# Kernel tuning notes

Measured on AMD Instinct MI355X. Metric: run time of the kernel, lower is better.

Reference implementation:

```python
import jax, jax.numpy as jnp
import numpy as np

C = 512
H_HEADS = 8
CTX_D = 768
GEO_D = 512
FFN_D = 4 * C
EPS = 1e-5


def _layernorm(x, g, b):
    mu = jnp.mean(x, axis=-1, keepdims=True)
    var = jnp.mean((x - mu) ** 2, axis=-1, keepdims=True)
    return (x - mu) * jax.lax.rsqrt(var + EPS) * g + b


def _cross_attn(x, ctx, Wq, Wk, Wv, Wo, bo, h):
    # x: (B, N, C), ctx: (B, S, Dctx)
    b, n, _ = x.shape
    s = ctx.shape[1]
    inner = Wq.shape[1]
    d = inner // h
    q = (x @ Wq).reshape(b, n, h, d)
    k = (ctx @ Wk).reshape(b, s, h, d)
    v = (ctx @ Wv).reshape(b, s, h, d)
    sim = jnp.einsum('bihd,bjhd->bhij', q, k) * (d ** -0.5)
    attn = jax.nn.softmax(sim, axis=-1)
    out = jnp.einsum('bhij,bjhd->bihd', attn, v).reshape(b, n, inner)
    return out @ Wo + bo


def setup_inputs() -> dict:
    key = jax.random.key(0)
    ks = jax.random.split(key, 24)
    std = lambda fan_in: 1.0 / np.sqrt(fan_in)
    inp = {
        'x': jax.random.normal(ks[0], (4, C, 64, 64), jnp.float32),
        'context': jax.random.normal(ks[1], (4, 77, CTX_D), jnp.float32),
        'geometry_tokens': jax.random.normal(ks[2], (4, 256, GEO_D), jnp.float32),
        # layernorm params (norm1..norm4)
        'g1': jnp.ones((C,)), 'b1': jnp.zeros((C,)),
        'g2': jnp.ones((C,)), 'b2': jnp.zeros((C,)),
        'g3': jnp.ones((C,)), 'b3': jnp.zeros((C,)),
        'g4': jnp.ones((C,)), 'b4': jnp.zeros((C,)),
        # cross-attention (context) weights
        'cWq': jax.random.normal(ks[3], (C, C)) * std(C),
        'cWk': jax.random.normal(ks[4], (CTX_D, C)) * std(CTX_D),
        'cWv': jax.random.normal(ks[5], (CTX_D, C)) * std(CTX_D),
        'cWo': jax.random.normal(ks[6], (C, C)) * std(C),
        'cbo': jnp.zeros((C,)),
        # geometry-attention weights
        'gWq': jax.random.normal(ks[7], (C, C)) * std(C),
        'gWk': jax.random.normal(ks[8], (GEO_D, C)) * std(GEO_D),
        'gWv': jax.random.normal(ks[9], (GEO_D, C)) * std(GEO_D),
        'gWo': jax.random.normal(ks[10], (C, C)) * std(C),
        'gbo': jnp.zeros((C,)),
        # FFN weights
        'W1': jax.random.normal(ks[11], (C, FFN_D)) * std(C),
        'bf1': jnp.zeros((FFN_D,)),
        'W2': jax.random.normal(ks[12], (FFN_D, C)) * std(FFN_D),
        'bf2': jnp.zeros((C,)),
    }
    return inp


def reference(x, context, geometry_tokens,
              g1, b1, g2, b2, g3, b3, g4, b4,
              cWq, cWk, cWv, cWo, cbo,
              gWq, gWk, gWv, gWo, gbo,
              W1, bf1, W2, bf2):
    b, c, h, w = x.shape
    t = x.reshape(b, c, h * w).transpose(0, 2, 1)  # (B, N, C)
    # self_attn is called with context=None -> identity, so this is t + norm1(t)
    t = t + _layernorm(t, g1, b1)
    t = t + _cross_attn(_layernorm(t, g2, b2), context, cWq, cWk, cWv, cWo, cbo, H_HEADS)
    t = t + _cross_attn(_layernorm(t, g3, b3), geometry_tokens, gWq, gWk, gWv, gWo, gbo, H_HEADS)
    hdn = jax.nn.gelu(_layernorm(t, g4, b4) @ W1 + bf1, approximate=False)
    t = t + hdn @ W2 + bf2
    return t.transpose(0, 2, 1).reshape(b, c, h, w)
```

## Files before the change

kernel.cpp:

```cpp
#include <hip/hip_runtime.h>
#include <hip/hip_bf16.h>

using bf16 = __hip_bfloat16;
typedef __attribute__((ext_vector_type(8))) short short8;
typedef __attribute__((ext_vector_type(4))) short short4v;
typedef __attribute__((ext_vector_type(4))) float floatx4;

#define DEVFN __device__ __forceinline__

DEVFN float bf2f(bf16 v) { return __bfloat162float(v); }
DEVFN bf16 f2bf(float v) { return __float2bfloat16(v); }
DEVFN float us2f(unsigned short u) {
    union { unsigned int i; float f; } c; c.i = ((unsigned int)u) << 16; return c.f;
}
DEVFN unsigned short f2bfbits(float v) {
    union { bf16 h; unsigned short u; } c; c.h = f2bf(v); return c.u;
}
DEVFN float loadF(const void* p, size_t i, int isf) {
    return isf ? ((const float*)p)[i] : us2f(((const unsigned short*)p)[i]);
}
DEVFN void gl_lds16(const bf16* g, short* l) {
    __builtin_amdgcn_global_load_lds(
        (const __attribute__((address_space(1))) unsigned int*)g,
        (__attribute__((address_space(3))) unsigned int*)l, 16, 0, 0);
}
DEVFN float fast_gelu(float v) {
    float u = v * (0.7978845608028654f + 0.0356774081f * v * v);
    float e = __expf(2.f * u);
    float th = 1.f - 2.f / (e + 1.f);
    return 0.5f * v * (1.f + th);
}

__global__ __launch_bounds__(256) void detect_kernel(const void* x, int* flag)
{
    __shared__ int any;
    if (threadIdx.x == 0) any = 0;
    __syncthreads();
    const unsigned short* p = (const unsigned short*)x;
    int hit = 0;
    for (int i = threadIdx.x; i < 8192; i += 256) {
        if ((p[i] & 0x7F80u) == 0x7F80u) hit = 1;
    }
    if (hit) any = 1;
    __syncthreads();
    if (threadIdx.x == 0) flag[0] = any;
}

struct CVTab {
    const void* src[14];
    bf16* dst[14];
    int cnt[14];
    int bstart[14];
};
__global__ __launch_bounds__(256) void convert_batch_kernel(
    CVTab tab, const int* __restrict__ flag)
{
    int isf = *flag;
    int b = blockIdx.x;
    int s = 0;
#pragma unroll
    for (int i = 1; i < 14; i++) if (b >= tab.bstart[i]) s = i;
    const void* src = tab.src[s];
    bf16* dst = tab.dst[s];
    int cnt = tab.cnt[s];
    int base = (b - tab.bstart[s]) * 2048;
    int lim = min(base + 2048, cnt);
    for (int i = base + (int)threadIdx.x; i < lim; i += 256)
        dst[i] = f2bf(loadF(src, i, isf));
}

__global__ __launch_bounds__(256) void ln_in_kernel(
    const void* __restrict__ x, float* __restrict__ t,
    const bf16* __restrict__ g, const bf16* __restrict__ bta,
    const int* __restrict__ flag, int NN)
{
    __shared__ float tile[16][516];
    int isf = *flag;
    int b = blockIdx.y;
    int n0 = blockIdx.x * 16;
    int tid = threadIdx.x;
    int nx = tid & 15, cy = tid >> 4;
#pragma unroll
    for (int p = 0; p < 32; p++) {
        int c = p * 16 + cy;
        tile[nx][c] = loadF(x, ((size_t)b * 512 + c) * NN + n0 + nx, isf);
    }
    __syncthreads();
    int w = tid >> 6, lane = tid & 63;
    for (int rr = 0; rr < 4; rr++) {
        int r = w * 4 + rr;
        float4 v0 = *(const float4*)&tile[r][lane * 8];
        float4 v1 = *(const float4*)&tile[r][lane * 8 + 4];
        float vals[8] = {v0.x, v0.y, v0.z, v0.w, v1.x, v1.y, v1.z, v1.w};
        float s = 0.f;
#pragma unroll
        for (int i = 0; i < 8; i++) s += vals[i];
#pragma unroll
        for (int off = 32; off; off >>= 1) s += __shfl_xor(s, off, 64);
        float mu = s * (1.f / 512.f);
        float sq = 0.f;
#pragma unroll
        for (int i = 0; i < 8; i++) { float d = vals[i] - mu; sq += d * d; }
#pragma unroll
        for (int off = 32; off; off >>= 1) sq += __shfl_xor(sq, off, 64);
        float rs = rsqrtf(sq * (1.f / 512.f) + 1e-5f);
        float out[8];
#pragma unroll
        for (int i = 0; i < 8; i++) {
            int c = lane * 8 + i;
            out[i] = vals[i] + (vals[i] - mu) * rs * bf2f(g[c]) + bf2f(bta[c]);
        }
        float* tp = t + ((size_t)b * NN + n0 + r) * 512 + lane * 8;
        *(float4*)tp = make_float4(out[0], out[1], out[2], out[3]);
        *(float4*)(tp + 4) = make_float4(out[4], out[5], out[6], out[7]);
    }
}

__global__ __launch_bounds__(256) void transpose_out_kernel(
    const float* __restrict__ t, const bf16* __restrict__ f,
    void* __restrict__ o, const int* __restrict__ flag,
    int C, int NN)
{
    __shared__ float tile[32][33];
    int isf = *flag;
    int b = blockIdx.z;
    int n0 = blockIdx.x * 32, c0 = blockIdx.y * 32;
    int tx = threadIdx.x, ty = threadIdx.y;
#pragma unroll
    for (int i = 0; i < 4; i++) {
        size_t idx = ((size_t)b * NN + n0 + ty + i * 8) * C + c0 + tx;
        tile[ty + i * 8][tx] = t[idx] + bf2f(f[idx]);
    }
    __syncthreads();
#pragma unroll
    for (int i = 0; i < 4; i++) {
        size_t oi = ((size_t)b * C + c0 + ty + i * 8) * NN + n0 + tx;
        float val = tile[tx][ty + i * 8];
        if (isf) ((float*)o)[oi] = val;
        else ((bf16*)o)[oi] = f2bf(val);
    }
}

struct TWTab {
    const void* src[10];
    bf16* dst[10];
    int K[10];
    int Nc[10];
    int tstart[10];
};
__global__ __launch_bounds__(256) void transpose_w_batch(
    TWTab tab, const int* __restrict__ flag)
{
    __shared__ float tile[32][33];
    int isf = *flag;
    int b = blockIdx.x;
    int s = 0;
#pragma unroll
    for (int i = 1; i < 10; i++) if (b >= tab.tstart[i]) s = i;
    const void* Wm = tab.src[s];
    bf16* WT = tab.dst[s];
    int K = tab.K[s], Nc = tab.Nc[s];
    int lt = b - tab.tstart[s];
    int ntx = Nc >> 5;
    int n0 = (lt % ntx) * 32, k0 = (lt / ntx) * 32;
    int tx = threadIdx.x, ty = threadIdx.y;
#pragma unroll
    for (int i = 0; i < 4; i++)
        tile[ty + i * 8][tx] = loadF(Wm, (size_t)(k0 + ty + i * 8) * Nc + n0 + tx, isf);
    __syncthreads();
#pragma unroll
    for (int i = 0; i < 4; i++)
        WT[(size_t)(n0 + ty + i * 8) * K + k0 + tx] = f2bf(tile[tx][ty + i * 8]);
}

__global__ __launch_bounds__(256) void ln_kernel(
    const float* __restrict__ t, const bf16* __restrict__ g, const bf16* __restrict__ bta,
    bf16* __restrict__ outp, int Mrows)
{
    int w = threadIdx.x >> 6, lane = threadIdx.x & 63;
    int row = blockIdx.x * 4 + w;
    if (row >= Mrows) return;
    const float* xr = t + (size_t)row * 512;
    float4 v0 = *(const float4*)(xr + lane * 8);
    float4 v1 = *(const float4*)(xr + lane * 8 + 4);
    float vals[8] = {v0.x, v0.y, v0.z, v0.w, v1.x, v1.y, v1.z, v1.w};
    float s = 0.f;
#pragma unroll
    for (int i = 0; i < 8; i++) s += vals[i];
#pragma unroll
    for (int off = 32; off; off >>= 1) s += __shfl_xor(s, off, 64);
    float mu = s * (1.f / 512.f);
    float sq = 0.f;
#pragma unroll
    for (int i = 0; i < 8; i++) { float d = vals[i] - mu; sq += d * d; }
#pragma unroll
    for (int off = 32; off; off >>= 1) sq += __shfl_xor(sq, off, 64);
    float rs = rsqrtf(sq * (1.f / 512.f) + 1e-5f);
#pragma unroll
    for (int i = 0; i < 8; i++) {
        int c = lane * 8 + i;
        float y = (vals[i] - mu) * rs * bf2f(g[c]) + bf2f(bta[c]);
        outp[(size_t)row * 512 + c] = f2bf(y);
    }
}

template <int MODE>
__global__ __launch_bounds__(256) void gemm64x2(
    const bf16* __restrict__ A,
    const bf16* __restrict__ WT0, const bf16* __restrict__ WT1,
    bf16* __restrict__ o0, bf16* __restrict__ o1,
    int M, int K, int Nc)
{
    const bf16* WT = blockIdx.z ? WT1 : WT0;
    bf16* outp = blockIdx.z ? o1 : o0;
    __shared__ short As[64 * 32];
    __shared__ short Bs[64 * 32];
    const int tid = threadIdx.x;
    const int m0 = blockIdx.y * 64;
    const int n0 = blockIdx.x * 64;
    const int w = tid >> 6;
    const int lane = tid & 63;
    const int lm = lane & 15;
    const int lq = lane >> 4;

    floatx4 acc[4];
#pragma unroll
    for (int nb = 0; nb < 4; nb++) acc[nb] = (floatx4){0.f, 0.f, 0.f, 0.f};

    const int srow = tid >> 2;
    const int scol = (tid & 3) << 3;
    const int agrow = m0 + srow;
    const bool aok = agrow < M;
    const bf16* Aptr = A + (size_t)agrow * K + scol;
    const bf16* Bptr = WT + (size_t)(n0 + srow) * K + scol;

    for (int k0 = 0; k0 < K; k0 += 32) {
        __syncthreads();
        int4 av = make_int4(0, 0, 0, 0);
        if (aok) av = *(const int4*)(Aptr + k0);
        *(int4*)(&As[srow * 32 + scol]) = av;
        *(int4*)(&Bs[srow * 32 + scol]) = *(const int4*)(Bptr + k0);
        __syncthreads();
        short8 a = *(const short8*)(&As[(w * 16 + lm) * 32 + lq * 8]);
#pragma unroll
        for (int nb = 0; nb < 4; nb++) {
            short8 b = *(const short8*)(&Bs[(nb * 16 + lm) * 32 + lq * 8]);
            acc[nb] = __builtin_amdgcn_mfma_f32_16x16x32_bf16(a, b, acc[nb], 0, 0, 0);
        }
    }

#pragma unroll
    for (int nb = 0; nb < 4; nb++) {
        int col = n0 + nb * 16 + lm;
#pragma unroll
        for (int r = 0; r < 4; r++) {
            int row = m0 + w * 16 + lq * 4 + r;
            if (row < M) {
                float v = acc[nb][r];
                if (MODE == 1) v = fast_gelu(v);
                outp[(size_t)row * Nc + col] = f2bf(v);
            }
        }
    }
}

#define MFMA_PAIR(RB, A00, A01, A10, A11)                                              \
    _Pragma("unroll")                                                                   \
    for (int cb = 0; cb < CB; cb++) {                                                   \
        acc[cb][RB]     = __builtin_amdgcn_mfma_f32_16x16x32_bf16(bf0[cb], A00, acc[cb][RB], 0, 0, 0);     \
        acc[cb][RB]     = __builtin_amdgcn_mfma_f32_16x16x32_bf16(bf1[cb], A01, acc[cb][RB], 0, 0, 0);     \
        acc[cb][RB + 1] = __builtin_amdgcn_mfma_f32_16x16x32_bf16(bf0[cb], A10, acc[cb][RB + 1], 0, 0, 0); \
        acc[cb][RB + 1] = __builtin_amdgcn_mfma_f32_16x16x32_bf16(bf1[cb], A11, acc[cb][RB + 1], 0, 0, 0); \
    }

template <int MODE, int CB>
__global__ __launch_bounds__(512, 2) void gemm8p(
    const bf16* __restrict__ A, const bf16* __restrict__ WT,
    const bf16* __restrict__ bias, void* __restrict__ outp,
    int K, int Nc)
{
    constexpr int BN = CB * 64;
    constexpr int ABUF = 256 * 64;
    constexpr int BBUF = BN * 64;
    __shared__ short As[2 * ABUF];
    __shared__ short Bs[2 * BBUF];

    const int tid = threadIdx.x;
    const int gx = gridDim.x;
    int g = blockIdx.y * gx + blockIdx.x;
    const int cpx = (gx * gridDim.y) >> 3;
    g = (g & 7) * cpx + (g >> 3);
    const int m0 = (g / gx) * 256;
    const int n0 = (g % gx) * BN;

    const int w = tid >> 6, lane = tid & 63;
    const int lm = lane & 15, lq = lane >> 4;
    const int wm = w >> 2, wn = w & 3;

    floatx4 acc[CB][8];
#pragma unroll
    for (int cb = 0; cb < CB; cb++)
#pragma unroll
        for (int rb = 0; rb < 8; rb++) acc[cb][rb] = (floatx4){0.f, 0.f, 0.f, 0.f};

    const int rbaseA = (tid >> 3) + ((tid >= 256) ? 96 : 0);
    const int chk = (((tid & 7) ^ ((tid >> 3) & 7)) << 3);
    const bf16* pA = A + (size_t)(m0 + rbaseA) * K + chk;
    const int rbaseB = ((tid >> 7) << (CB == 4 ? 6 : 5)) + ((tid >> 3) & 15);
    const bf16* pB = WT + (size_t)(n0 + rbaseB) * K + chk;
    const int wbA = w * 512 + ((w >= 4) ? 6144 : 0);
    const int wbB = (CB == 4) ? ((w >> 1) * 4096 + (w & 1) * 512)
                              : ((w >> 1) * 2048 + (w & 1) * 512);
    const size_t K32 = (size_t)K * 32;
    const size_t K16 = (size_t)K * 16;

    const int arow = (wm * 128 + lm) * 64;
    const int brow = (wn * CB * 16 + lm) * 64;
    const int sl0 = ((lq ^ (lm & 7)) << 3);
    const int sl1 = (((4 + lq) ^ (lm & 7)) << 3);

    const int nt = K >> 6;

#pragma unroll
    for (int q = 0; q < 4; q++) gl_lds16(pA + (size_t)q * K32, As + q * 2048 + wbA);
    if constexpr (CB == 4) {
        gl_lds16(pB,           Bs + wbB);
        gl_lds16(pB + K16,     Bs + 1024 + wbB);
        gl_lds16(pB + 2 * K16, Bs + 2048 + wbB);
        gl_lds16(pB + 3 * K16, Bs + 3072 + wbB);
    } else {
        gl_lds16(pB,       Bs + wbB);
        gl_lds16(pB + K16, Bs + 1024 + wbB);
    }
    {
        const bf16* qA = pA + 64;
        const bf16* qB = pB + 64;
        if constexpr (CB == 4) {
            gl_lds16(qB,           Bs + BBUF + wbB);
            gl_lds16(qB + K16,     Bs + BBUF + 1024 + wbB);
            gl_lds16(qB + 2 * K16, Bs + BBUF + 2048 + wbB);
            gl_lds16(qB + 3 * K16, Bs + BBUF + 3072 + wbB);
            gl_lds16(qA,           As + ABUF + wbA);
            gl_lds16(qA + K32,     As + ABUF + 2048 + wbA);
            asm volatile("s_waitcnt vmcnt(6)\n\ts_barrier" ::: "memory");
        } else {
            gl_lds16(qB,           Bs + BBUF + wbB);
            gl_lds16(qB + K16, Bs + BBUF + 1024 + wbB);
            gl_lds16(qA,           As + ABUF + wbA);
            gl_lds16(qA + K32,     As + ABUF + 2048 + wbA);
            gl_lds16(qA + 2 * K32, As + ABUF + 4096 + wbA);
            asm volatile("s_waitcnt vmcnt(5)\n\ts_barrier" ::: "memory");
        }
    }

    for (int s = 0; s < nt; ++s) {
        const int cu = s & 1;
        const short* cA = As + cu * ABUF;
        const short* cB = Bs + cu * BBUF;
        short* oA = As + (cu ^ 1) * ABUF;
        short* sA = As + cu * ABUF;
        short* sB = Bs + cu * BBUF;
        const bf16* pA1 = pA + (s + 1) * 64;
        const bf16* pA2 = pA + (s + 2) * 64;
        const bf16* pB2 = pB + (s + 2) * 64;
        short8 bf0[CB], bf1[CB], x0, x1, y0, y1;

#pragma unroll
        for (int cb = 0; cb < CB; cb++) {
            bf0[cb] = *(const short8*)&cB[brow + cb * 1024 + sl0];
            bf1[cb] = *(const short8*)&cB[brow + cb * 1024 + sl1];
        }
        x0 = *(const short8*)&cA[arow + sl0];
        x1 = *(const short8*)&cA[arow + sl1];
        y0 = *(const short8*)&cA[arow + 1024 + sl0];
        y1 = *(const short8*)&cA[arow + 1024 + sl1];
        if (s + 1 < nt) {
            if constexpr (CB == 4) {
                gl_lds16(pA1 + 2 * K32, oA + 2 * 2048 + wbA);
                gl_lds16(pA1 + 3 * K32, oA + 3 * 2048 + wbA);
            } else {
                gl_lds16(pA1 + 3 * K32, oA + 3 * 2048 + wbA);
            }
        }
        asm volatile("s_barrier" ::: "memory");
        __builtin_amdgcn_s_setprio(1);
        MFMA_PAIR(0, x0, x1, y0, y1)
        __builtin_amdgcn_s_setprio(0);
        asm volatile("s_waitcnt lgkmcnt(0)\n\ts_barrier" ::: "memory");

        x0 = *(const short8*)&cA[arow + 2 * 1024 + sl0];
        x1 = *(const short8*)&cA[arow + 2 * 1024 + sl1];
        y0 = *(const short8*)&cA[arow + 3 * 1024 + sl0];
        y1 = *(const short8*)&cA[arow + 3 * 1024 + sl1];
        if (s + 2 < nt) {
            gl_lds16(pB2,       sB + wbB);
            gl_lds16(pB2 + K16, sB + 1024 + wbB);
        }
        asm volatile("s_barrier" ::: "memory");
        __builtin_amdgcn_s_setprio(1);
        MFMA_PAIR(2, x0, x1, y0, y1)
        __builtin_amdgcn_s_setprio(0);
        asm volatile("s_waitcnt lgkmcnt(0)\n\ts_barrier" ::: "memory");

        x0 = *(const short8*)&cA[arow + 4 * 1024 + sl0];
        x1 = *(const short8*)&cA[arow + 4 * 1024 + sl1];
        y0 = *(const short8*)&cA[arow + 5 * 1024 + sl0];
        y1 = *(const short8*)&cA[arow + 5 * 1024 + sl1];
        if (s + 2 < nt) {
            if constexpr (CB == 4) {
                gl_lds16(pB2 + 2 * K16, sB + 2048 + wbB);
                gl_lds16(pB2 + 3 * K16, sB + 3072 + wbB);
            } else {
                gl_lds16(pA2, sA + wbA);
            }
        }
        asm volatile("s_barrier" ::: "memory");
        __builtin_amdgcn_s_setprio(1);
        MFMA_PAIR(4, x0, x1, y0, y1)
        __builtin_amdgcn_s_setprio(0);
        asm volatile("s_waitcnt lgkmcnt(0)\n\ts_barrier" ::: "memory");

        x0 = *(const short8*)&cA[arow + 6 * 1024 + sl0];
        x1 = *(const short8*)&cA[arow + 6 * 1024 + sl1];
        y0 = *(const short8*)&cA[arow + 7 * 1024 + sl0];
        y1 = *(const short8*)&cA[arow + 7 * 1024 + sl1];
        if (s + 2 < nt) {
            if constexpr (CB == 4) {
                gl_lds16(pA2,       sA + wbA);
                gl_lds16(pA2 + K32, sA + 2048 + wbA);
            } else {
                gl_lds16(pA2 + K32,     sA + 2048 + wbA);
                gl_lds16(pA2 + 2 * K32, sA + 4096 + wbA);
            }
        }
        asm volatile("s_barrier" ::: "memory");
        __builtin_amdgcn_s_setprio(1);
        MFMA_PAIR(6, x0, x1, y0, y1)
        __builtin_amdgcn_s_setprio(0);
        if (s <= nt - 3) {
            if constexpr (CB == 4)
                asm volatile("s_waitcnt vmcnt(6) lgkmcnt(0)\n\ts_barrier" ::: "memory");
            else
                asm volatile("s_waitcnt vmcnt(5) lgkmcnt(0)\n\ts_barrier" ::: "memory");
        } else if (s == nt - 2) {
            asm volatile("s_waitcnt vmcnt(0) lgkmcnt(0)\n\ts_barrier" ::: "memory");
        } else {
            asm volatile("s_waitcnt lgkmcnt(0)\n\ts_barrier" ::: "memory");
        }
    }
    __syncthreads();

    float4 bias4[CB];
#pragma unroll
    for (int cb = 0; cb < CB; cb++) {
        if (bias) {
            const bf16* bp = bias + n0 + wn * (CB * 16) + cb * 16 + lq * 4;
            bias4[cb] = make_float4(bf2f(bp[0]), bf2f(bp[1]), bf2f(bp[2]), bf2f(bp[3]));
        } else {
            bias4[cb] = make_float4(0.f, 0.f, 0.f, 0.f);
        }
    }

    if constexpr (MODE == 2) {
        float* po = (float*)outp;
#pragma unroll
        for (int rb = 0; rb < 8; rb++) {
            size_t m = m0 + wm * 128 + rb * 16 + lm;
#pragma unroll
            for (int cb = 0; cb < CB; cb++) {
                float* p = po + m * Nc + n0 + wn * (CB * 16) + cb * 16 + lq * 4;
                float4 f = *(float4*)p;
                f.x += acc[cb][rb][0] + bias4[cb].x;
                f.y += acc[cb][rb][1] + bias4[cb].y;
                f.z += acc[cb][rb][2] + bias4[cb].z;
                f.w += acc[cb][rb][3] + bias4[cb].w;
                *(float4*)p = f;
            }
        }
    } else if constexpr (CB == 2) {
        unsigned short* op = (unsigned short*)outp;
#pragma unroll
        for (int rb = 0; rb < 8; rb++) {
            size_t m = m0 + wm * 128 + rb * 16 + lm;
#pragma unroll
            for (int cb = 0; cb < 2; cb++) {
                short4v pk;
#pragma unroll
                for (int r = 0; r < 4; r++) {
                    float vv = acc[cb][rb][r] + ((const float*)&bias4[cb])[r];
                    if (MODE == 1) vv = fast_gelu(vv);
                    pk[r] = (short)f2bfbits(vv);
                }
                *(short4v*)(op + m * Nc + n0 + wn * 32 + cb * 16 + lq * 4) = pk;
            }
        }
    } else {
        unsigned short* stgb = (unsigned short*)&As[w * 1024];
        unsigned short* op = (unsigned short*)outp;
#pragma unroll
        for (int rb = 0; rb < 8; rb++) {
#pragma unroll
            for (int cb = 0; cb < 4; cb++) {
                short4v pk;
#pragma unroll
                for (int r = 0; r < 4; r++) {
                    float vv = acc[cb][rb][r] + ((const float*)&bias4[cb])[r];
                    if (MODE == 1) vv = fast_gelu(vv);
                    pk[r] = (short)f2bfbits(vv);
                }
                int chunk = (cb * 2 + (lq >> 1)) ^ (lm & 7);
                *(short4v*)(&stgb[lm * 64 + chunk * 8 + (lq & 1) * 4]) = pk;
            }
#pragma unroll
            for (int p = 0; p < 2; p++) {
                int row = p * 8 + (lane >> 3);
                int chunk = lane & 7;
                short8 ov = *(const short8*)(&stgb[row * 64 + ((chunk ^ (row & 7)) * 8)]);
                size_t m = m0 + wm * 128 + rb * 16 + row;
                *(short8*)(op + m * Nc + n0 + wn * 64 + chunk * 8) = ov;
            }
        }
    }
}

template <int SPAD, int SVALID>
__global__ __launch_bounds__(256) void attn_mfma_kernel(
    const bf16* __restrict__ q, const bf16* __restrict__ k, const bf16* __restrict__ v,
    bf16* __restrict__ o, int N)
{
    constexpr int MB = SPAD / 16;
    constexpr int KS = SPAD / 32;
    __shared__ unsigned short lds[SPAD * 64 + 64 * SPAD];
    unsigned short* Ks = lds;
    unsigned short* Vt = lds + SPAD * 64;
    unsigned short* Pw = lds;

    const int tid = threadIdx.x;
    const int b = blockIdx.x >> 3;
    const int h = blockIdx.x & 7;
    const int n0 = blockIdx.y * 64;
    const int w = tid >> 6, lane = tid & 63;
    const int lm = lane & 15, lq = lane >> 4;

    const unsigned short* kp = (const unsigned short*)k;
    const unsigned short* vp = (const unsigned short*)v;
    for (int idx = tid * 8; idx < SPAD * 64; idx += 2048) {
        int s = idx >> 6, d0 = idx & 63;
        short8 kv = {0, 0, 0, 0, 0, 0, 0, 0};
        short8 vv = {0, 0, 0, 0, 0, 0, 0, 0};
        if (s < SVALID) {
            size_t gb = ((size_t)(b * SVALID + s)) * 512 + h * 64 + d0;
            kv = *(const short8*)(kp + gb);
            vv = *(const short8*)(vp + gb);
        }
        int kc = (d0 >> 3) ^ (s & 7);
        *(short8*)(&Ks[s * 64 + kc * 8]) = kv;
        const unsigned short* vvp = (const unsigned short*)&vv;
#pragma unroll
        for (int i = 0; i < 8; i++) {
            int d = d0 + i;
            int sc = (s >> 3) ^ (d & 7);
            Vt[d * SPAD + sc * 8 + (s & 7)] = vvp[i];
        }
    }

    const int q0 = n0 + w * 16;
    const unsigned short* qp = (const unsigned short*)q;
    size_t qbase = ((size_t)(b * N + q0 + lm)) * 512 + h * 64 + lq * 8;
    short8 qf0 = *(const short8*)(qp + qbase);
    short8 qf1 = *(const short8*)(qp + qbase + 32);
    __syncthreads();

    floatx4 sacc[MB];
#pragma unroll
    for (int mb = 0; mb < MB; mb++) sacc[mb] = (floatx4){0.f, 0.f, 0.f, 0.f};
#pragma unroll
    for (int mb = 0; mb < MB; mb++) {
        int srow = mb * 16 + lm;
        short8 a0 = *(const short8*)(&Ks[srow * 64 + ((lq ^ (lm & 7)) * 8)]);
        short8 a1 = *(const short8*)(&Ks[srow * 64 + (((4 + lq) ^ (lm & 7)) * 8)]);
        sacc[mb] = __builtin_amdgcn_mfma_f32_16x16x32_bf16(a0, qf0, sacc[mb], 0, 0, 0);
        sacc[mb] = __builtin_amdgcn_mfma_f32_16x16x32_bf16(a1, qf1, sacc[mb], 0, 0, 0);
    }

    float mx = -1e30f;
#pragma unroll
    for (int mb = 0; mb < MB; mb++)
#pragma unroll
        for (int r = 0; r < 4; r++) {
            int s = mb * 16 + lq * 4 + r;
            if (s < SVALID) mx = fmaxf(mx, sacc[mb][r]);
        }
    mx = fmaxf(mx, __shfl_xor(mx, 16, 64));
    mx = fmaxf(mx, __shfl_xor(mx, 32, 64));
    mx *= 0.125f;
    float sum = 0.f;
#pragma unroll
    for (int mb = 0; mb < MB; mb++)
#pragma unroll
        for (int r = 0; r < 4; r++) {
            int s = mb * 16 + lq * 4 + r;
            float e = (s < SVALID) ? __expf(sacc[mb][r] * 0.125f - mx) : 0.f;
            sacc[mb][r] = e;
            sum += e;
        }
    sum += __shfl_xor(sum, 16, 64);
    sum += __shfl_xor(sum, 32, 64);
    float inv = 1.f / sum;

    __syncthreads();

    unsigned short* Pme = Pw + w * 16 * SPAD;
#pragma unroll
    for (int mb = 0; mb < MB; mb++) {
        short4v pk;
        pk[0] = (short)f2bfbits(sacc[mb][0] * inv);
        pk[1] = (short)f2bfbits(sacc[mb][1] * inv);
        pk[2] = (short)f2bfbits(sacc[mb][2] * inv);
        pk[3] = (short)f2bfbits(sacc[mb][3] * inv);
        int chunk = (mb * 2 + (lq >> 1)) ^ (lm & 7);
        *(short4v*)(&Pme[lm * SPAD + chunk * 8 + (lq & 1) * 4]) = pk;
    }

    floatx4 oacc[4];
#pragma unroll
    for (int mb2 = 0; mb2 < 4; mb2++) oacc[mb2] = (floatx4){0.f, 0.f, 0.f, 0.f};
    for (int ks = 0; ks < KS; ks++) {
        int sch = ((ks * 4 + lq) ^ (lm & 7)) * 8;
        short8 bfrag = *(const short8*)(&Pme[lm * SPAD + sch]);
#pragma unroll
        for (int mb2 = 0; mb2 < 4; mb2++) {
            int d = mb2 * 16 + lm;
            short8 afrag = *(const short8*)(&Vt[d * SPAD + sch]);
            oacc[mb2] = __builtin_amdgcn_mfma_f32_16x16x32_bf16(afrag, bfrag, oacc[mb2], 0, 0, 0);
        }
    }

#pragma unroll
    for (int mb2 = 0; mb2 < 4; mb2++) {
        short4v ok;
        ok[0] = (short)f2bfbits(oacc[mb2][0]);
        ok[1] = (short)f2bfbits(oacc[mb2][1]);
        ok[2] = (short)f2bfbits(oacc[mb2][2]);
        ok[3] = (short)f2bfbits(oacc[mb2][3]);
        int chunk = (mb2 * 2 + (lq >> 1)) ^ (lm & 7);
        *(short4v*)(&Pme[lm * 64 + chunk * 8 + (lq & 1) * 4]) = ok;
    }
    unsigned short* op = (unsigned short*)o;
#pragma unroll
    for (int p = 0; p < 2; p++) {
        int row = p * 8 + (lane >> 3);
        int chunk = lane & 7;
        short8 ov = *(const short8*)(&Pme[row * 64 + ((chunk ^ (row & 7)) * 8)]);
        *(short8*)(op + ((size_t)(b * N + n0 + w * 16 + row)) * 512 + h * 64 + chunk * 8) = ov;
    }
}

extern "C" void kernel_launch(void* const* d_in, const int* in_sizes, int n_in,
                              void* d_out, int out_size, void* d_ws, size_t ws_size,
                              hipStream_t stream)
{
    const void* x   = d_in[0];
    const void* ctx = d_in[1];
    const void* geo = d_in[2];
    const void* g1 = d_in[3];  const void* b1 = d_in[4];
    const void* g2 = d_in[5];  const void* b2 = d_in[6];
    const void* g3 = d_in[7];  const void* b3 = d_in[8];
    const void* g4 = d_in[9];  const void* b4 = d_in[10];
    const void* cWq = d_in[11]; const void* cWk = d_in[12];
    const void* cWv = d_in[13]; const void* cWo = d_in[14];
    const void* cbo = d_in[15];
    const void* gWq = d_in[16]; const void* gWk = d_in[17];
    const void* gWv = d_in[18]; const void* gWo = d_in[19];
    const void* gbo = d_in[20];
    const void* W1 = d_in[21];  const void* bf1 = d_in[22];
    const void* W2 = d_in[23];  const void* bf2 = d_in[24];

    const int B = 4, C = 512, NN = 4096;
    const int M = B * NN;

    char* ws = (char*)d_ws;
    size_t off = 0;
    auto alloc = [&](size_t bytes) -> void* {
        void* p = ws + off; off += (bytes + 255) & ~(size_t)255; return p;
    };
    int*   flag = (int*)alloc(256);
    float* t  = (float*)alloc((size_t)M * C * 4);
    bf16* u   = (bf16*)alloc((size_t)M * C * 2);
    bf16* qb  = (bf16*)alloc((size_t)M * C * 2);
    bf16* fb  = (bf16*)alloc((size_t)M * C * 2);
    bf16* kb  = (bf16*)alloc((size_t)B * 256 * C * 2);
    bf16* vb  = (bf16*)alloc((size_t)B * 256 * C * 2);
    bf16* ctxb = (bf16*)alloc((size_t)B * 77 * 768 * 2);
    bf16* geob = (bf16*)alloc((size_t)B * 256 * 512 * 2);
    bf16* cWqT = (bf16*)alloc((size_t)512 * 512 * 2);
    bf16* cWkT = (bf16*)alloc((size_t)512 * 768 * 2);
    bf16* cWvT = (bf16*)alloc((size_t)512 * 768 * 2);
    bf16* cWoT = (bf16*)alloc((size_t)512 * 512 * 2);
    bf16* gWqT = (bf16*)alloc((size_t)512 * 512 * 2);
    bf16* gWkT = (bf16*)alloc((size_t)512 * 512 * 2);
    bf16* gWvT = (bf16*)alloc((size_t)512 * 512 * 2);
    bf16* gWoT = (bf16*)alloc((size_t)512 * 512 * 2);
    bf16* W1T  = (bf16*)alloc((size_t)2048 * 512 * 2);
    bf16* W2T  = (bf16*)alloc((size_t)512 * 2048 * 2);
    bf16* prm  = (bf16*)alloc((size_t)7680 * 2);
    bf16* ob = u;

    int chunk;
    bf16* hb;
    size_t rem = (ws_size > off) ? (ws_size - off) : 0;
    if (rem >= (size_t)16384 * 2048 * 2) { chunk = 16384; hb = (bf16*)alloc((size_t)16384 * 2048 * 2); }
    else if (rem >= (size_t)8192 * 2048 * 2) { chunk = 8192; hb = (bf16*)alloc((size_t)8192 * 2048 * 2); }
    else { chunk = 4096; hb = qb; }
    (void)in_sizes; (void)n_in; (void)out_size;

    bf16 *pg1 = prm, *pb1 = prm + 512, *pg2 = prm + 1024, *pb2 = prm + 1536;
    bf16 *pg3 = prm + 2048, *pb3 = prm + 2560, *pg4 = prm + 3072, *pb4 = prm + 3584;
    bf16 *pcbo = prm + 4096, *pgbo = prm + 4608, *pbf1 = prm + 5120, *pbf2 = prm + 7168;

    dim3 tb(32, 8);

    detect_kernel<<<1, 256, 0, stream>>>(x, flag);

    {
        CVTab cv;
        const void* csrc[14] = {g1, b1, g2, b2, g3, b3, g4, b4, cbo, gbo, bf1, bf2, ctx, geo};
        bf16* cdst[14] = {prm, prm + 512, prm + 1024, prm + 1536, prm + 2048, prm + 2560,
                          prm + 3072, prm + 3584, prm + 4096, prm + 4608, prm + 5120,
                          prm + 7168, ctxb, geob};
        int ccnt[14] = {512, 512, 512, 512, 512, 512, 512, 512, 512, 512, 2048, 512,
                        B * 77 * 768, B * 256 * 512};
        int bacc = 0;
        for (int i = 0; i < 14; i++) {
            cv.src[i] = csrc[i]; cv.dst[i] = cdst[i]; cv.cnt[i] = ccnt[i];
            cv.bstart[i] = bacc;
            bacc += (ccnt[i] + 2047) / 2048;
        }
        convert_batch_kernel<<<bacc, 256, 0, stream>>>(cv, flag);
    }

    ln_in_kernel<<<dim3(NN / 16, B), 256, 0, stream>>>(x, t, pg1, pb1, flag, NN);

    {
        TWTab tw;
        const void* wsrc[10] = {cWq, cWk, cWv, cWo, gWq, gWk, gWv, gWo, W1, W2};
        bf16* wdst[10] = {cWqT, cWkT, cWvT, cWoT, gWqT, gWkT, gWvT, gWoT, W1T, W2T};
        int wK[10]  = {512, 768, 768, 512, 512, 512, 512, 512, 512, 2048};
        int wNc[10] = {512, 512, 512, 512, 512, 512, 512, 512, 2048, 512};
        int tacc = 0;
        for (int i = 0; i < 10; i++) {
            tw.src[i] = wsrc[i]; tw.dst[i] = wdst[i]; tw.K[i] = wK[i]; tw.Nc[i] = wNc[i];
            tw.tstart[i] = tacc;
            tacc += (wNc[i] / 32) * (wK[i] / 32);
        }
        transpose_w_batch<<<tacc, tb, 0, stream>>>(tw, flag);
    }

    ln_kernel<<<M / 4, 256, 0, stream>>>(t, pg2, pb2, u, M);
    gemm8p<0, 2><<<dim3(4, M / 256), 512, 0, stream>>>(u, cWqT, nullptr, qb, 512, 512);
    gemm64x2<0><<<dim3(8, (308 + 63) / 64, 2), 256, 0, stream>>>(ctxb, cWkT, cWvT, kb, vb, 308, 768, 512);
    attn_mfma_kernel<128, 77><<<dim3(B * 8, NN / 64), 256, 0, stream>>>(qb, kb, vb, ob, NN);
    gemm8p<2, 2><<<dim3(4, M / 256), 512, 0, stream>>>(ob, cWoT, pcbo, t, 512, 512);

    ln_kernel<<<M / 4, 256, 0, stream>>>(t, pg3, pb3, u, M);
    gemm8p<0, 2><<<dim3(4, M / 256), 512, 0, stream>>>(u, gWqT, nullptr, qb, 512, 512);
    gemm64x2<0><<<dim3(8, 1024 / 64, 2), 256, 0, stream>>>(geob, gWkT, gWvT, kb, vb, 1024, 512, 512);
    attn_mfma_kernel<256, 256><<<dim3(B * 8, NN / 64), 256, 0, stream>>>(qb, kb, vb, ob, NN);
    gemm8p<2, 2><<<dim3(4, M / 256), 512, 0, stream>>>(ob, gWoT, pgbo, t, 512, 512);

    ln_kernel<<<M / 4, 256, 0, stream>>>(t, pg4, pb4, u, M);
    for (int mc = 0; mc < M / chunk; mc++) {
        bf16* uc = u + (size_t)mc * chunk * 512;
        bf16* fc = fb + (size_t)mc * chunk * 512;
        gemm8p<1, 4><<<dim3(2048 / 256, chunk / 256), 512, 0, stream>>>(uc, W1T, pbf1, hb, 512, 2048);
        gemm8p<0, 2><<<dim3(512 / 128, chunk / 256), 512, 0, stream>>>(hb, W2T, pbf2, fc, 2048, 512);
    }

    transpose_out_kernel<<<dim3(NN / 32, C / 32, B), tb, 0, stream>>>(t, fb, d_out, flag, C, NN);
}
```

Baseline: 472.0 us.

## Fuse norm2 into input kernel and defer residual adds into layernorm kernels

The second layernorm is computed inside the input-transpose kernel, which removes one full pass over the fp32 residual. The attention output projections now write bf16 results to separate buffers (rc, rg) rather than read-modify-writing the fp32 residual in the GEMM epilogue. Later layernorms and the final transpose sum these buffers on the fly. This trades fp32 RMW traffic for extra bf16 reads, adds two extra M×C buffers, and rounds residual contributions to bf16, which changes precision.

```diff
diff --git a/kernel.cpp b/kernel.cpp
--- a/kernel.cpp
+++ b/kernel.cpp
@@ -71,7 +71,9 @@
 
 __global__ __launch_bounds__(256) void ln_in_kernel(
     const void* __restrict__ x, float* __restrict__ t,
-    const bf16* __restrict__ g, const bf16* __restrict__ bta,
+    const bf16* __restrict__ g1c, const bf16* __restrict__ b1c,
+    const bf16* __restrict__ g2c, const bf16* __restrict__ b2c,
+    bf16* __restrict__ u,
     const int* __restrict__ flag, int NN)
 {
     __shared__ float tile[16][516];
@@ -108,16 +110,85 @@
 #pragma unroll
         for (int i = 0; i < 8; i++) {
             int c = lane * 8 + i;
-            out[i] = vals[i] + (vals[i] - mu) * rs * bf2f(g[c]) + bf2f(bta[c]);
-        }
-        float* tp = t + ((size_t)b * NN + n0 + r) * 512 + lane * 8;
+            out[i] = vals[i] + (vals[i] - mu) * rs * bf2f(g1c[c]) + bf2f(b1c[c]);
+        }
+        size_t rbase = ((size_t)b * NN + n0 + r) * 512 + lane * 8;
+        float* tp = t + rbase;
         *(float4*)tp = make_float4(out[0], out[1], out[2], out[3]);
         *(float4*)(tp + 4) = make_float4(out[4], out[5], out[6], out[7]);
-    }
+        float s2 = 0.f;
+#pragma unroll
+        for (int i = 0; i < 8; i++) s2 += out[i];
+#pragma unroll
+        for (int off = 32; off; off >>= 1) s2 += __shfl_xor(s2, off, 64);
+        float mu2 = s2 * (1.f / 512.f);
+        float sq2 = 0.f;
+#pragma unroll
+        for (int i = 0; i < 8; i++) { float d = out[i] - mu2; sq2 += d * d; }
+#pragma unroll
+        for (int off = 32; off; off >>= 1) sq2 += __shfl_xor(sq2, off, 64);
+        float rs2 = rsqrtf(sq2 * (1.f / 512.f) + 1e-5f);
+        short4v uo[2];
+#pragma unroll
+        for (int i = 0; i < 8; i++) {
+            int c = lane * 8 + i;
+            uo[i >> 2][i & 3] =
+                (short)f2bfbits((out[i] - mu2) * rs2 * bf2f(g2c[c]) + bf2f(b2c[c]));
+        }
+        *(short4v*)((unsigned short*)u + rbase) = uo[0];
+        *(short4v*)((unsigned short*)u + rbase + 4) = uo[1];
+    }
+}
+
+__global__ __launch_bounds__(256) void ln_res_kernel(
+    const float* __restrict__ t, const bf16* __restrict__ r1,
+    const bf16* __restrict__ r2,
+    const bf16* __restrict__ g, const bf16* __restrict__ bta,
+    bf16* __restrict__ outp, int Mrows)
+{
+    int w = threadIdx.x >> 6, lane = threadIdx.x & 63;
+    int row = blockIdx.x * 4 + w;
+    if (row >= Mrows) return;
+    size_t base = (size_t)row * 512 + lane * 8;
+    float4 v0 = *(const float4*)(t + base);
+    float4 v1 = *(const float4*)(t + base + 4);
+    float vals[8] = {v0.x, v0.y, v0.z, v0.w, v1.x, v1.y, v1.z, v1.w};
+    {
+        short8 a = *(const short8*)((const unsigned short*)r1 + base);
+#pragma unroll
+        for (int i = 0; i < 8; i++) vals[i] += us2f(((unsigned short*)&a)[i]);
+    }
+    if (r2) {
+        short8 a = *(const short8*)((const unsigned short*)r2 + base);
+#pragma unroll
+        for (int i = 0; i < 8; i++) vals[i] += us2f(((unsigned short*)&a)[i]);
+    }
+    float s = 0.f;
+#pragma unroll
+    for (int i = 0; i < 8; i++) s += vals[i];
+#pragma unroll
+    for (int off = 32; off; off >>= 1) s += __shfl_xor(s, off, 64);
+    float mu = s * (1.f / 512.f);
+    float sq = 0.f;
+#pragma unroll
+    for (int i = 0; i < 8; i++) { float d = vals[i] - mu; sq += d * d; }
+#pragma unroll
+    for (int off = 32; off; off >>= 1) sq += __shfl_xor(sq, off, 64);
+    float rs = rsqrtf(sq * (1.f / 512.f) + 1e-5f);
+    short4v uo[2];
+#pragma unroll
+    for (int i = 0; i < 8; i++) {
+        int c = lane * 8 + i;
+        uo[i >> 2][i & 3] =
+            (short)f2bfbits((vals[i] - mu) * rs * bf2f(g[c]) + bf2f(bta[c]));
+    }
+    *(short4v*)((unsigned short*)outp + base) = uo[0];
+    *(short4v*)((unsigned short*)outp + base + 4) = uo[1];
 }
 
 __global__ __launch_bounds__(256) void transpose_out_kernel(
-    const float* __restrict__ t, const bf16* __restrict__ f,
+    const float* __restrict__ t, const bf16* __restrict__ rc,
+    const bf16* __restrict__ rg, const bf16* __restrict__ f,
     void* __restrict__ o, const int* __restrict__ flag,
     int C, int NN)
 {
@@ -129,7 +200,7 @@
 #pragma unroll
     for (int i = 0; i < 4; i++) {
         size_t idx = ((size_t)b * NN + n0 + ty + i * 8) * C + c0 + tx;
-        tile[ty + i * 8][tx] = t[idx] + bf2f(f[idx]);
+        tile[ty + i * 8][tx] = t[idx] + bf2f(rc[idx]) + bf2f(rg[idx]) + bf2f(f[idx]);
     }
     __syncthreads();
 #pragma unroll
@@ -171,37 +242,6 @@
 #pragma unroll
     for (int i = 0; i < 4; i++)
         WT[(size_t)(n0 + ty + i * 8) * K + k0 + tx] = f2bf(tile[tx][ty + i * 8]);
-}
-
-__global__ __launch_bounds__(256) void ln_kernel(
-    const float* __restrict__ t, const bf16* __restrict__ g, const bf16* __restrict__ bta,
-    bf16* __restrict__ outp, int Mrows)
-{
-    int w = threadIdx.x >> 6, lane = threadIdx.x & 63;
-    int row = blockIdx.x * 4 + w;
-    if (row >= Mrows) return;
-    const float* xr = t + (size_t)row * 512;
-    float4 v0 = *(const float4*)(xr + lane * 8);
-    float4 v1 = *(const float4*)(xr + lane * 8 + 4);
-    float vals[8] = {v0.x, v0.y, v0.z, v0.w, v1.x, v1.y, v1.z, v1.w};
-    float s = 0.f;
-#pragma unroll
-    for (int i = 0; i < 8; i++) s += vals[i];
-#pragma unroll
-    for (int off = 32; off; off >>= 1) s += __shfl_xor(s, off, 64);
-    float mu = s * (1.f / 512.f);
-    float sq = 0.f;
-#pragma unroll
-    for (int i = 0; i < 8; i++) { float d = vals[i] - mu; sq += d * d; }
-#pragma unroll
-    for (int off = 32; off; off >>= 1) sq += __shfl_xor(sq, off, 64);
-    float rs = rsqrtf(sq * (1.f / 512.f) + 1e-5f);
-#pragma unroll
-    for (int i = 0; i < 8; i++) {
-        int c = lane * 8 + i;
-        float y = (vals[i] - mu) * rs * bf2f(g[c]) + bf2f(bta[c]);
-        outp[(size_t)row * 512 + c] = f2bf(y);
-    }
 }
 
 template <int MODE>
@@ -688,6 +728,8 @@
     float* t  = (float*)alloc((size_t)M * C * 4);
     bf16* u   = (bf16*)alloc((size_t)M * C * 2);
     bf16* qb  = (bf16*)alloc((size_t)M * C * 2);
+    bf16* rc  = (bf16*)alloc((size_t)M * C * 2);
+    bf16* rg  = (bf16*)alloc((size_t)M * C * 2);
     bf16* fb  = (bf16*)alloc((size_t)M * C * 2);
     bf16* kb  = (bf16*)alloc((size_t)B * 256 * C * 2);
     bf16* vb  = (bf16*)alloc((size_t)B * 256 * C * 2);
@@ -739,7 +781,7 @@
         convert_batch_kernel<<<bacc, 256, 0, stream>>>(cv, flag);
     }
 
-    ln_in_kernel<<<dim3(NN / 16, B), 256, 0, stream>>>(x, t, pg1, pb1, flag, NN);
+    ln_in_kernel<<<dim3(NN / 16, B), 256, 0, stream>>>(x, t, pg1, pb1, pg2, pb2, u, flag, NN);
 
     {
         TWTab tw;
@@ -756,19 +798,18 @@
         transpose_w_batch<<<tacc, tb, 0, stream>>>(tw, flag);
     }
 
-    ln_kernel<<<M / 4, 256, 0, stream>>>(t, pg2, pb2, u, M);
     gemm8p<0, 2><<<dim3(4, M / 256), 512, 0, stream>>>(u, cWqT, nullptr, qb, 512, 512);
     gemm64x2<0><<<dim3(8, (308 + 63) / 64, 2), 256, 0, stream>>>(ctxb, cWkT, cWvT, kb, vb, 308, 768, 512);
     attn_mfma_kernel<128, 77><<<dim3(B * 8, NN / 64), 256, 0, stream>>>(qb, kb, vb, ob, NN);
-    gemm8p<2, 2><<<dim3(4, M / 256), 512, 0, stream>>>(ob, cWoT, pcbo, t, 512, 512);
-
-    ln_kernel<<<M / 4, 256, 0, stream>>>(t, pg3, pb3, u, M);
+    gemm8p<0, 2><<<dim3(4, M / 256), 512, 0, stream>>>(ob, cWoT, pcbo, rc, 512, 512);
+    ln_res_kernel<<<M / 4, 256, 0, stream>>>(t, rc, nullptr, pg3, pb3, u, M);
+
     gemm8p<0, 2><<<dim3(4, M / 256), 512, 0, stream>>>(u, gWqT, nullptr, qb, 512, 512);
     gemm64x2<0><<<dim3(8, 1024 / 64, 2), 256, 0, stream>>>(geob, gWkT, gWvT, kb, vb, 1024, 512, 512);
     attn_mfma_kernel<256, 256><<<dim3(B * 8, NN / 64), 256, 0, stream>>>(qb, kb, vb, ob, NN);
-    gemm8p<2, 2><<<dim3(4, M / 256), 512, 0, stream>>>(ob, gWoT, pgbo, t, 512, 512);
-
-    ln_kernel<<<M / 4, 256, 0, stream>>>(t, pg4, pb4, u, M);
+    gemm8p<0, 2><<<dim3(4, M / 256), 512, 0, stream>>>(ob, gWoT, pgbo, rg, 512, 512);
+    ln_res_kernel<<<M / 4, 256, 0, stream>>>(t, rc, rg, pg4, pb4, u, M);
+
     for (int mc = 0; mc < M / chunk; mc++) {
         bf16* uc = u + (size_t)mc * chunk * 512;
         bf16* fc = fb + (size_t)mc * chunk * 512;
@@ -776,5 +817,5 @@
         gemm8p<0, 2><<<dim3(512 / 128, chunk / 256), 512, 0, stream>>>(hb, W2T, pbf2, fc, 2048, 512);
     }
 
-    transpose_out_kernel<<<dim3(NN / 32, C / 32, B), tb, 0, stream>>>(t, fb, d_out, flag, C, NN);
-}
+    transpose_out_kernel<<<dim3(NN / 32, C / 32, B), tb, 0, stream>>>(t, rc, rg, fb, d_out, flag, C, NN);
+}
```

Result: no change. 470.1 us (-0.4%).
